# Optimization experiments

Measured on AMD Instinct MI355X. Metric: run time of the kernel, lower is better.

The kernel has to match this reference:

```python
import jax, jax.numpy as jnp
import numpy as np
import math

B, S, D = 4, 2048, 768
H, DH = 12, 64  # num heads, head dim; H*DH == D


def setup_inputs() -> dict:
    key = jax.random.key(0)
    ks = jax.random.split(key, 10)
    q = jax.random.normal(ks[0], (B, S, D), jnp.float32)
    k = jax.random.normal(ks[1], (B, S, D), jnp.float32)
    v = jax.random.normal(ks[2], (B, S, D), jnp.float32)
    attention_mask = jax.random.bernoulli(ks[3], 0.1, (B, S, S))
    s = 1.0 / math.sqrt(D)
    # Linear weights stored as [in, out] so projection is x @ W + b
    Wq = jax.random.uniform(ks[4], (D, D), jnp.float32, -s, s)
    bq = jax.random.uniform(ks[5], (D,), jnp.float32, -s, s)
    Wk = jax.random.uniform(ks[6], (D, D), jnp.float32, -s, s)
    bk = jax.random.uniform(ks[7], (D,), jnp.float32, -s, s)
    Wv = jax.random.uniform(ks[8], (D, D), jnp.float32, -s, s)
    bv = jax.random.uniform(ks[9], (D,), jnp.float32, -s, s)
    return {"q": q, "k": k, "v": v, "attention_mask": attention_mask,
            "Wq": Wq, "bq": bq, "Wk": Wk, "bk": bk, "Wv": Wv, "bv": bv}


def _split_heads(x):
    # [B, S, D] -> [B, H, S, DH]
    return x.reshape(B, -1, H, DH).transpose(0, 2, 1, 3)


def reference(q, k, v, attention_mask, Wq, bq, Wk, bk, Wv, bv):
    Q = _split_heads(q @ Wq + bq)
    K = _split_heads(k @ Wk + bk)
    V = _split_heads(v @ Wv + bv)
    scores = jnp.einsum('bhqd,bhkd->bhqk', Q, K) / math.sqrt(DH)
    # masked_fill(mask, -1e9); 3-dim mask broadcasts over heads
    scores = jnp.where(attention_mask[:, None, :, :], -1.0e9, scores)
    probs = jax.nn.softmax(scores, axis=-1)
    ctx = jnp.einsum('bhqk,bhkd->bhqd', probs, V)
    ctx = ctx.transpose(0, 2, 1, 3).reshape(B, -1, H * DH)
    return ctx, probs
```

## Files before the change

kernel.cpp:

```cpp
#include <hip/hip_runtime.h>
#include <hip/hip_bf16.h>

#define BB 4
#define SS 2048
#define DD 768
#define HH 12
#define NE 6291456

typedef unsigned short u16t;
typedef unsigned char  u8t;
typedef unsigned int   u32t;
typedef __attribute__((ext_vector_type(8)))  short bf16x8;
typedef __attribute__((ext_vector_type(4)))  float f32x4;

union FragU { bf16x8 v; ushort4 h[2]; uint4 u; u32t g[4]; };

__device__ __forceinline__ u16t f2bf(float f) {
  union { float fv; u32t u; } x; x.fv = f;
  u32t r = x.u + 0x7FFFu + ((x.u >> 16) & 1u);
  return (u16t)(r >> 16);
}

__device__ __forceinline__ u32t pkbf2(float a, float b) {
  __hip_bfloat162 h2 = __float22bfloat162_rn(make_float2(a, b));
  union { __hip_bfloat162 h; u32t u; } c; c.h = h2;
  return c.u;
}

__device__ __forceinline__ u32t pack4(u32t w) {
  return ((w & 0x01010101u) * 0x01020408u) >> 24;
}
__device__ __forceinline__ u32t pack16b(uint4 v) {
  return pack4(v.x) | (pack4(v.y) << 4) | (pack4(v.z) << 8) | (pack4(v.w) << 12);
}
__device__ __forceinline__ u32t pack_i4(int4 v) {
  return (v.x ? 1u : 0u) | ((v.y ? 1u : 0u) << 1) | ((v.z ? 1u : 0u) << 2) | ((v.w ? 1u : 0u) << 3);
}
__device__ __forceinline__ u32t pack_f4(float4 v) {
  return (v.x != 0.f ? 1u : 0u) | ((v.y != 0.f ? 1u : 0u) << 1) |
         ((v.z != 0.f ? 1u : 0u) << 2) | ((v.w != 0.f ? 1u : 0u) << 3);
}

__global__ void detect_kernel(const u32t* __restrict__ mp, int* __restrict__ flag)
{
  __shared__ int s_isb, s_isf;
  if (threadIdx.x == 0) { s_isb = 0; s_isf = 0; }
  __syncthreads();
  int isb = 0, isf = 0;
  for (int i = threadIdx.x; i < 16384; i += 256) {
    u32t v = mp[i];
    if ((v & 0xFF000000u) == 0x3F000000u) isf = 1;
    else if (v & 0xFFFFFF00u) isb = 1;
  }
  if (isb) atomicOr(&s_isb, 1);
  if (isf) atomicOr(&s_isf, 1);
  __syncthreads();
  if (threadIdx.x == 0) *flag = s_isf ? 2 : (s_isb ? 1 : 0);
}

__global__ __launch_bounds__(256)
void mask_pack_kernel(const void* __restrict__ msk, const int* __restrict__ flagp,
                      u32t* __restrict__ pm)
{
  const int gid = blockIdx.x * 256 + threadIdx.x;
  const int row = gid >> 6, c = gid & 63;
  const int fmt = *flagp;
  const size_t src = (size_t)(row >> 11) * SS * SS + (size_t)(row & 2047) * SS + c * 32;
  u32t bits;
  if (fmt == 1) {
    const uint4* s = (const uint4*)((const u8t*)msk + src);
    bits = pack16b(s[0]) | (pack16b(s[1]) << 16);
  } else if (fmt == 0) {
    const int4* s = (const int4*)((const int*)msk + src);
    bits = 0;
#pragma unroll
    for (int j = 0; j < 8; ++j) bits |= pack_i4(s[j]) << (j * 4);
  } else {
    const float4* s = (const float4*)((const float*)msk + src);
    bits = 0;
#pragma unroll
    for (int j = 0; j < 8; ++j) bits |= pack_f4(s[j]) << (j * 4);
  }
  pm[(size_t)row * 64 + c] = bits;
}

__global__ __launch_bounds__(256)
void cvt_x_kernel(const float* __restrict__ q, const float* __restrict__ k,
                  const float* __restrict__ v, u16t* __restrict__ xb)
{
  const float* src = (blockIdx.y == 0) ? q : (blockIdx.y == 1) ? k : v;
  u16t* dst = xb + (size_t)blockIdx.y * NE;
  const size_t i = ((size_t)blockIdx.x * 256 + threadIdx.x) * 8;
  float4 f0 = *(const float4*)(src + i);
  float4 f1 = *(const float4*)(src + i + 4);
  uint4 o;
  o.x = pkbf2(f0.x, f0.y); o.y = pkbf2(f0.z, f0.w);
  o.z = pkbf2(f1.x, f1.y); o.w = pkbf2(f1.z, f1.w);
  *(uint4*)(dst + i) = o;
}

__global__ __launch_bounds__(256)
void cvt_w_kernel(const float* __restrict__ Wq, const float* __restrict__ Wk,
                  const float* __restrict__ Wv, u16t* __restrict__ Wt)
{
  __shared__ u16t T[64 * 72];
  const int t = threadIdx.x;
  const float* W = (blockIdx.z == 0) ? Wq : (blockIdx.z == 1) ? Wk : Wv;
  u16t* wt = Wt + (size_t)blockIdx.z * DD * DD;
  const int n0 = blockIdx.x * 64, k0 = blockIdx.y * 64;
  const int r = t >> 2, cs = (t & 3) * 16;
#pragma unroll
  for (int i = 0; i < 4; ++i) {
    float4 f = *(const float4*)(W + (size_t)(k0 + r) * DD + n0 + cs + i * 4);
    T[(cs + i * 4 + 0) * 72 + r] = f2bf(f.x);
    T[(cs + i * 4 + 1) * 72 + r] = f2bf(f.y);
    T[(cs + i * 4 + 2) * 72 + r] = f2bf(f.z);
    T[(cs + i * 4 + 3) * 72 + r] = f2bf(f.w);
  }
  __syncthreads();
#pragma unroll
  for (int i = 0; i < 2; ++i) {
    uint4 vv = *(const uint4*)&T[r * 72 + cs + i * 8];
    *(uint4*)(wt + (size_t)(n0 + r) * DD + k0 + cs + i * 8) = vv;
  }
}

__device__ __forceinline__ void proj_core(const u16t* __restrict__ Xrow,
    const u16t* __restrict__ Wrow, u16t* __restrict__ Ab, u16t* __restrict__ Bb,
    int t, f32x4 acc[8])
{
  const int w = t >> 6, l = t & 63;
  const int lq = l & 15, lg = l >> 4;
  const int gr = l >> 3;
  const int gc = ((l & 7) ^ (l >> 3)) * 8;

#define PSTAGE_A(kk_, buf_)                                                       \
  _Pragma("unroll")                                                               \
  for (int j = 0; j < 2; ++j) {                                                   \
    const int rr = (w * 2 + j) * 8 + gr;                                          \
    const u16t* gsrc = Xrow + (size_t)rr * DD + (kk_) + gc;                       \
    __builtin_amdgcn_global_load_lds(                                             \
        (const __attribute__((address_space(1))) void*)gsrc,                      \
        (__attribute__((address_space(3))) void*)(Ab + (buf_) * 4096 + (w * 2 + j) * 512), \
        16, 0, 0);                                                                \
  }
#define PSTAGE_B(kk_, buf_)                                                       \
  _Pragma("unroll")                                                               \
  for (int j = 0; j < 4; ++j) {                                                   \
    const int rr = (w * 4 + j) * 8 + gr;                                          \
    const u16t* gsrc = Wrow + (size_t)rr * DD + (kk_) + gc;                       \
    __builtin_amdgcn_global_load_lds(                                             \
        (const __attribute__((address_space(1))) void*)gsrc,                      \
        (__attribute__((address_space(3))) void*)(Bb + (buf_) * 8192 + (w * 4 + j) * 512), \
        16, 0, 0);                                                                \
  }

  PSTAGE_A(0, 0)
  PSTAGE_B(0, 0)
  __syncthreads();

  const int xa = (lq & 7) * 8;
  for (int kki = 0; kki < 12; ++kki) {
    const int buf = kki & 1;
    if (kki < 11) { PSTAGE_A((kki + 1) * 64, buf ^ 1) PSTAGE_B((kki + 1) * 64, buf ^ 1) }
    const int arow = w * 16 + lq;
    FragU af[2];
#pragma unroll
    for (int ks = 0; ks < 2; ++ks) {
      af[ks].h[0] = *(const ushort4*)&Ab[buf * 4096 + arow * 64 + ((ks * 32 + 4 * lg) ^ xa)];
      af[ks].h[1] = *(const ushort4*)&Ab[buf * 4096 + arow * 64 + ((ks * 32 + 4 * lg + 16) ^ xa)];
    }
#pragma unroll
    for (int nt = 0; nt < 8; ++nt) {
      const int brow = nt * 16 + lq;
#pragma unroll
      for (int ks = 0; ks < 2; ++ks) {
        FragU bf;
        bf.h[0] = *(const ushort4*)&Bb[buf * 8192 + brow * 64 + ((ks * 32 + 4 * lg) ^ xa)];
        bf.h[1] = *(const ushort4*)&Bb[buf * 8192 + brow * 64 + ((ks * 32 + 4 * lg + 16) ^ xa)];
        acc[nt] = __builtin_amdgcn_mfma_f32_16x16x32_bf16(af[ks].v, bf.v, acc[nt], 0, 0, 0);
      }
    }
    __syncthreads();
  }
#undef PSTAGE_A
#undef PSTAGE_B
}

__global__ __launch_bounds__(256, 3)
void proj_all_kernel(const u16t* __restrict__ Xb, const u16t* __restrict__ Wt,
                     const float* __restrict__ bq, const float* __restrict__ bk,
                     const float* __restrict__ bv,
                     u16t* __restrict__ Qb, u16t* __restrict__ Kb, u16t* __restrict__ Vb)
{
  __shared__ u16t Ab[2 * 4096];
  __shared__ u16t Bb[2 * 8192];
  const int t = threadIdx.x;
  const int w = t >> 6, l = t & 63;
  const int lq = l & 15, lg = l >> 4;
  const int m0 = blockIdx.x * 64;
  const int n0 = blockIdx.y * 128;
  const int z = blockIdx.z;
  const int b = m0 >> 11;

  const float* bias = (z == 0) ? bq : (z == 1) ? bk : bv;
  u16t* out = (z == 0) ? Qb : (z == 1) ? Kb : Vb;

  f32x4 acc[8];
#pragma unroll
  for (int i = 0; i < 8; ++i)
#pragma unroll
    for (int r = 0; r < 4; ++r) acc[i][r] = 0.f;

  proj_core(Xb + (size_t)z * NE + (size_t)m0 * DD,
            Wt + (size_t)z * DD * DD + (size_t)n0 * DD, Ab, Bb, t, acc);

  if (z < 2) {
#pragma unroll
    for (int nt = 0; nt < 8; ++nt) {
      const int n = n0 + nt * 16 + lq;
      const int h = n >> 6, dh = n & 63;
      const float bb = bias[n];
#pragma unroll
      for (int r = 0; r < 4; ++r) {
        const int s = (m0 & 2047) + w * 16 + 4 * lg + r;
        out[((size_t)(b * HH + h) * SS + s) * 64 + dh] = f2bf(acc[nt][r] + bb);
      }
    }
  } else {
    u16t* Tl = Bb;
#pragma unroll
    for (int nt = 0; nt < 8; ++nt) {
      const float bb = bias[n0 + nt * 16 + lq];
#pragma unroll
      for (int r = 0; r < 4; ++r)
        Tl[(nt * 16 + lq) * 72 + w * 16 + 4 * lg + r] = f2bf(acc[nt][r] + bb);
    }
    __syncthreads();
    const int rowl = t >> 1;
    const int half = t & 1;
    const int ncol = n0 + rowl;
    const int h = ncol >> 6, dh = ncol & 63;
    const int s = (m0 & 2047) + half * 32;
    u16t* dst = out + ((size_t)(b * HH + h) * 64 + dh) * SS + s;
#pragma unroll
    for (int i = 0; i < 4; ++i) {
      uint4 vv = *(const uint4*)&Tl[rowl * 72 + half * 32 + i * 8];
      *(uint4*)(dst + i * 8) = vv;
    }
  }
}

__global__ __launch_bounds__(256, 4)
void attn_kernel(const u16t* __restrict__ Qh, const u16t* __restrict__ Kh,
                 const u16t* __restrict__ Vh, const u32t* __restrict__ pm,
                 float* __restrict__ ctx, float* __restrict__ probs)
{
  __shared__ u16t KV[4][64 * 64];

  const int t = threadIdx.x;
  const int w = t >> 6, l = t & 63;
  const int lq = l & 15, lg = l >> 4;

  const int bid = (int)blockIdx.x;
  const int lid = (bid & 7) * 192 + (bid >> 3);
  const int bh = lid >> 5;
  const int qt = lid & 31;
  const int b = bh / HH;
  const int qbase = qt * 64 + w * 16;

  const u16t* qh = Qh + (size_t)bh * SS * 64;
  const u16t* kh = Kh + (size_t)bh * SS * 64;
  const u16t* vh = Vh + (size_t)bh * SS * 64;

  FragU bq_[2];
  {
    const u16t* qp = qh + (size_t)(qbase + lq) * 64;
#pragma unroll
    for (int ks = 0; ks < 2; ++ks) {
      bq_[ks].h[0] = *(const ushort4*)(qp + ks * 32 + 4 * lg);
      bq_[ks].h[1] = *(const ushort4*)(qp + ks * 32 + 4 * lg + 16);
    }
  }

  const u32t* mrow = pm + ((size_t)b * SS + qbase + lq) * 64;

  const float SC = 0.125f * 1.44269504f;
  const float B4 = 4.0f * 1.44269504f;

  const int gr = l >> 3;
  const int gc = ((l & 7) ^ (l >> 3)) * 8;

#define STAGE_K(kt_, slot_)                                                       \
  _Pragma("unroll")                                                               \
  for (int j = 0; j < 2; ++j) {                                                   \
    const int rr = (w * 2 + j) * 8 + gr;                                          \
    const u16t* gsrc = kh + (size_t)((kt_) * 64 + rr) * 64 + gc;                  \
    __builtin_amdgcn_global_load_lds(                                             \
        (const __attribute__((address_space(1))) void*)gsrc,                      \
        (__attribute__((address_space(3))) void*)(&KV[slot_][(w * 2 + j) * 512]), \
        16, 0, 0);                                                                \
  }

#define STAGE_V(kt_, vbuf_)                                                       \
  _Pragma("unroll")                                                               \
  for (int j = 0; j < 2; ++j) {                                                   \
    const int dv = (w * 2 + j) * 8 + gr;                                          \
    const u16t* gsrc = vh + (size_t)dv * SS + (kt_) * 64 + gc;                    \
    __builtin_amdgcn_global_load_lds(                                             \
        (const __attribute__((address_space(1))) void*)gsrc,                      \
        (__attribute__((address_space(3))) void*)(&KV[2 + (vbuf_)][(w * 2 + j) * 512]), \
        16, 0, 0);                                                                \
  }

#define QKT_CHUNK(nt_, slot_, accv)                                               \
  {                                                                               \
    const int krow = (nt_) * 16 + lq;                                             \
    const int xr = (lq & 7) * 8;                                                  \
    _Pragma("unroll")                                                             \
    for (int r = 0; r < 4; ++r) (accv)[r] = 0.f;                                  \
    _Pragma("unroll")                                                             \
    for (int ks = 0; ks < 2; ++ks) {                                              \
      FragU ak;                                                                   \
      ak.h[0] = *(const ushort4*)&KV[slot_][krow * 64 + ((ks * 32 + 4 * lg) ^ xr)]; \
      ak.h[1] = *(const ushort4*)&KV[slot_][krow * 64 + ((ks * 32 + 4 * lg + 16) ^ xr)]; \
      (accv) = __builtin_amdgcn_mfma_f32_16x16x32_bf16(ak.v, bq_[ks].v, (accv), 0, 0, 0); \
    }                                                                             \
  }

#define COMPUTE1(slot_, mw_)                                                      \
  {                                                                               \
    _Pragma("unroll")                                                             \
    for (int nt = 0; nt < 4; ++nt) {                                              \
      f32x4 a;                                                                    \
      QKT_CHUNK(nt, slot_, a)                                                     \
      const u32t word = (nt < 2) ? (mw_).x : (mw_).y;                             \
      const int sh = 16 * (nt & 1) + 4 * lg;                                      \
      _Pragma("unroll")                                                           \
      for (int r = 0; r < 4; ++r) {                                               \
        float s = fmaf(a[r], SC, -B4);                                            \
        if ((word >> (sh + r)) & 1) s = -1.0e9f;                                  \
        ssum += __builtin_exp2f(s);                                               \
      }                                                                           \
    }                                                                             \
  }

  float ssum = 0.f;

  STAGE_K(0, 0)
  uint2 mA = *(const uint2*)(mrow + 0);
  STAGE_K(1, 1)
  uint2 mB = *(const uint2*)(mrow + 2);

  for (int kt = 0; kt < 32; kt += 2) {
    if (kt == 0) { asm volatile("s_waitcnt vmcnt(0)" ::: "memory"); }
    else         { asm volatile("s_waitcnt vmcnt(3)" ::: "memory"); }
    __builtin_amdgcn_s_barrier();
    {
      uint2 mw = mA;
      if (kt < 30) { STAGE_K(kt + 2, (kt + 2) % 3) mA = *(const uint2*)(mrow + (kt + 2) * 2); }
      COMPUTE1(kt % 3, mw)
    }
    if (kt == 0 || kt == 30) { asm volatile("s_waitcnt vmcnt(0)" ::: "memory"); }
    else                     { asm volatile("s_waitcnt vmcnt(3)" ::: "memory"); }
    __builtin_amdgcn_s_barrier();
    {
      uint2 mw = mB;
      if (kt < 30) { STAGE_K(kt + 3, (kt + 3) % 3) mB = *(const uint2*)(mrow + (kt + 3) * 2); }
      COMPUTE1((kt + 1) % 3, mw)
    }
  }

  ssum += __shfl_xor(ssum, 16);
  ssum += __shfl_xor(ssum, 32);
  const float inv = 1.0f / ssum;

  f32x4 acco[4];
#pragma unroll
  for (int i = 0; i < 4; ++i)
#pragma unroll
    for (int r = 0; r < 4; ++r) acco[i][r] = 0.f;

  const size_t prow = ((size_t)bh * SS + qbase + lq) * SS;

  __builtin_amdgcn_s_barrier();
  STAGE_K(0, 0) STAGE_V(0, 0)
  uint2 mw2 = *(const uint2*)(mrow + 0);

  for (int kt = 0; kt < 32; ++kt) {
    const int buf = kt & 1;
    if (kt == 0) { asm volatile("s_waitcnt vmcnt(0)" ::: "memory"); }
    else         { asm volatile("s_waitcnt vmcnt(4)" ::: "memory"); }
    __builtin_amdgcn_s_barrier();
    uint2 mw = mw2;
    if (kt < 31) {
      STAGE_K(kt + 1, buf ^ 1) STAGE_V(kt + 1, buf ^ 1)
      mw2 = *(const uint2*)(mrow + (kt + 1) * 2);
    }

    f32x4 sc[4];
#pragma unroll
    for (int nt = 0; nt < 4; ++nt) {
      f32x4 a;
      QKT_CHUNK(nt, buf, a)
      const u32t word = (nt < 2) ? mw.x : mw.y;
      const int sh = 16 * (nt & 1) + 4 * lg;
#pragma unroll
      for (int r = 0; r < 4; ++r) {
        float s = fmaf(a[r], SC, -B4);
        if ((word >> (sh + r)) & 1) s = -1.0e9f;
        sc[nt][r] = __builtin_exp2f(s) * inv;
      }
    }

#pragma unroll
    for (int nt = 0; nt < 4; ++nt) {
      __builtin_nontemporal_store(sc[nt], (f32x4*)(probs + prow + kt * 64 + nt * 16 + 4 * lg));
    }

    FragU pf[2];
#pragma unroll
    for (int c = 0; c < 2; ++c) {
      pf[c].g[0] = pkbf2(sc[2 * c][0],     sc[2 * c][1]);
      pf[c].g[1] = pkbf2(sc[2 * c][2],     sc[2 * c][3]);
      pf[c].g[2] = pkbf2(sc[2 * c + 1][0], sc[2 * c + 1][1]);
      pf[c].g[3] = pkbf2(sc[2 * c + 1][2], sc[2 * c + 1][3]);
    }

    __builtin_amdgcn_s_setprio(1);
#pragma unroll
    for (int c = 0; c < 2; ++c) {
#pragma unroll
      for (int n0 = 0; n0 < 4; ++n0) {
        const int dv = n0 * 16 + lq;
        const int xv = (lq & 7) * 8;
        FragU bvv;
        bvv.h[0] = *(const ushort4*)&KV[2 + buf][dv * 64 + ((c * 32 + 4 * lg) ^ xv)];
        bvv.h[1] = *(const ushort4*)&KV[2 + buf][dv * 64 + ((c * 32 + 4 * lg + 16) ^ xv)];
        acco[n0] = __builtin_amdgcn_mfma_f32_16x16x32_bf16(pf[c].v, bvv.v, acco[n0], 0, 0, 0);
      }
    }
    __builtin_amdgcn_s_setprio(0);
  }

  {
    const int h = bh % HH;
    const size_t cbase = (size_t)(b * SS + qbase) * DD + h * 64;
#pragma unroll
    for (int n0 = 0; n0 < 4; ++n0)
#pragma unroll
      for (int r = 0; r < 4; ++r)
        ctx[cbase + (size_t)(4 * lg + r) * DD + n0 * 16 + lq] = acco[n0][r];
  }
#undef STAGE_K
#undef STAGE_V
#undef QKT_CHUNK
#undef COMPUTE1
}

extern "C" void kernel_launch(void* const* d_in, const int* in_sizes, int n_in,
                              void* d_out, int out_size, void* d_ws, size_t ws_size,
                              hipStream_t stream)
{
  const float* q   = (const float*)d_in[0];
  const float* k   = (const float*)d_in[1];
  const float* v   = (const float*)d_in[2];
  const void*  msk = d_in[3];
  const float* Wq  = (const float*)d_in[4];
  const float* bq  = (const float*)d_in[5];
  const float* Wk  = (const float*)d_in[6];
  const float* bk  = (const float*)d_in[7];
  const float* Wv  = (const float*)d_in[8];
  const float* bv  = (const float*)d_in[9];
  (void)in_sizes; (void)n_in; (void)out_size; (void)ws_size;

  u16t* Qb = (u16t*)d_ws;
  u16t* Kb = Qb + NE;
  u16t* Vb = Kb + NE;
  u32t* pm = (u32t*)(Vb + NE);
  int* flag = (int*)(pm + (size_t)BB * SS * 64);

  float* ctx   = (float*)d_out;
  float* probs = ctx + NE;

  u16t* Xb = (u16t*)probs;
  u16t* Wt = Xb + (size_t)3 * NE;

  detect_kernel<<<1, 256, 0, stream>>>((const u32t*)msk, flag);
  mask_pack_kernel<<<2048, 256, 0, stream>>>(msk, flag, pm);

  cvt_x_kernel<<<dim3(3072, 3), 256, 0, stream>>>(q, k, v, Xb);
  cvt_w_kernel<<<dim3(12, 12, 3), 256, 0, stream>>>(Wq, Wk, Wv, Wt);

  proj_all_kernel<<<dim3(BB * SS / 64, DD / 128, 3), 256, 0, stream>>>(
      Xb, Wt, bq, bk, bv, Qb, Kb, Vb);

  attn_kernel<<<dim3(1536), 256, 0, stream>>>(Qb, Kb, Vb, pm, ctx, probs);
}
```

Before: 382.8 us.

## Split attention into separate row-sum and PV kernels, use regular probs stores

Splits the single attention kernel into two launches. The first computes the softmax denominators using a 3-slot K-only LDS buffer and writes inverse sums to workspace. The second reloads them and does the normalized probs write plus the PV matmul. The intent is to let each kernel use fewer resources or schedule better, at the cost of an extra launch and a small global round trip for the sums. The probs stores also change from nontemporal to regular stores.

```diff
diff --git a/kernel.cpp b/kernel.cpp
--- a/kernel.cpp
+++ b/kernel.cpp
@@ -251,12 +251,12 @@
   }
 }
 
+
 __global__ __launch_bounds__(256, 4)
-void attn_kernel(const u16t* __restrict__ Qh, const u16t* __restrict__ Kh,
-                 const u16t* __restrict__ Vh, const u32t* __restrict__ pm,
-                 float* __restrict__ ctx, float* __restrict__ probs)
-{
-  __shared__ u16t KV[4][64 * 64];
+void attn_sum_kernel(const u16t* __restrict__ Qh, const u16t* __restrict__ Kh,
+                     const u32t* __restrict__ pm, float* __restrict__ invb)
+{
+  __shared__ u16t KV[3][64 * 64];
 
   const int t = threadIdx.x;
   const int w = t >> 6, l = t & 63;
@@ -271,7 +271,6 @@
 
   const u16t* qh = Qh + (size_t)bh * SS * 64;
   const u16t* kh = Kh + (size_t)bh * SS * 64;
-  const u16t* vh = Vh + (size_t)bh * SS * 64;
 
   FragU bq_[2];
   {
@@ -284,14 +283,12 @@
   }
 
   const u32t* mrow = pm + ((size_t)b * SS + qbase + lq) * 64;
-
   const float SC = 0.125f * 1.44269504f;
   const float B4 = 4.0f * 1.44269504f;
-
   const int gr = l >> 3;
   const int gc = ((l & 7) ^ (l >> 3)) * 8;
 
-#define STAGE_K(kt_, slot_)                                                       \
+#define STAGE_K1(kt_, slot_)                                                      \
   _Pragma("unroll")                                                               \
   for (int j = 0; j < 2; ++j) {                                                   \
     const int rr = (w * 2 + j) * 8 + gr;                                          \
@@ -302,18 +299,7 @@
         16, 0, 0);                                                                \
   }
 
-#define STAGE_V(kt_, vbuf_)                                                       \
-  _Pragma("unroll")                                                               \
-  for (int j = 0; j < 2; ++j) {                                                   \
-    const int dv = (w * 2 + j) * 8 + gr;                                          \
-    const u16t* gsrc = vh + (size_t)dv * SS + (kt_) * 64 + gc;                    \
-    __builtin_amdgcn_global_load_lds(                                             \
-        (const __attribute__((address_space(1))) void*)gsrc,                      \
-        (__attribute__((address_space(3))) void*)(&KV[2 + (vbuf_)][(w * 2 + j) * 512]), \
-        16, 0, 0);                                                                \
-  }
-
-#define QKT_CHUNK(nt_, slot_, accv)                                               \
+#define QKT1(nt_, slot_, accv)                                                    \
   {                                                                               \
     const int krow = (nt_) * 16 + lq;                                             \
     const int xr = (lq & 7) * 8;                                                  \
@@ -333,7 +319,7 @@
     _Pragma("unroll")                                                             \
     for (int nt = 0; nt < 4; ++nt) {                                              \
       f32x4 a;                                                                    \
-      QKT_CHUNK(nt, slot_, a)                                                     \
+      QKT1(nt, slot_, a)                                                          \
       const u32t word = (nt < 2) ? (mw_).x : (mw_).y;                             \
       const int sh = 16 * (nt & 1) + 4 * lg;                                      \
       _Pragma("unroll")                                                           \
@@ -347,9 +333,9 @@
 
   float ssum = 0.f;
 
-  STAGE_K(0, 0)
+  STAGE_K1(0, 0)
   uint2 mA = *(const uint2*)(mrow + 0);
-  STAGE_K(1, 1)
+  STAGE_K1(1, 1)
   uint2 mB = *(const uint2*)(mrow + 2);
 
   for (int kt = 0; kt < 32; kt += 2) {
@@ -358,7 +344,7 @@
     __builtin_amdgcn_s_barrier();
     {
       uint2 mw = mA;
-      if (kt < 30) { STAGE_K(kt + 2, (kt + 2) % 3) mA = *(const uint2*)(mrow + (kt + 2) * 2); }
+      if (kt < 30) { STAGE_K1(kt + 2, (kt + 2) % 3) mA = *(const uint2*)(mrow + (kt + 2) * 2); }
       COMPUTE1(kt % 3, mw)
     }
     if (kt == 0 || kt == 30) { asm volatile("s_waitcnt vmcnt(0)" ::: "memory"); }
@@ -366,14 +352,97 @@
     __builtin_amdgcn_s_barrier();
     {
       uint2 mw = mB;
-      if (kt < 30) { STAGE_K(kt + 3, (kt + 3) % 3) mB = *(const uint2*)(mrow + (kt + 3) * 2); }
+      if (kt < 30) { STAGE_K1(kt + 3, (kt + 3) % 3) mB = *(const uint2*)(mrow + (kt + 3) * 2); }
       COMPUTE1((kt + 1) % 3, mw)
     }
   }
 
   ssum += __shfl_xor(ssum, 16);
   ssum += __shfl_xor(ssum, 32);
-  const float inv = 1.0f / ssum;
+  if (lg == 0)
+    invb[(size_t)bh * SS + qbase + lq] = 1.0f / ssum;
+#undef STAGE_K1
+#undef QKT1
+#undef COMPUTE1
+}
+
+__global__ __launch_bounds__(256, 4)
+void attn_pv_kernel(const u16t* __restrict__ Qh, const u16t* __restrict__ Kh,
+                    const u16t* __restrict__ Vh, const u32t* __restrict__ pm,
+                    const float* __restrict__ invb,
+                    float* __restrict__ ctx, float* __restrict__ probs)
+{
+  __shared__ u16t KV[4][64 * 64];
+
+  const int t = threadIdx.x;
+  const int w = t >> 6, l = t & 63;
+  const int lq = l & 15, lg = l >> 4;
+
+  const int bid = (int)blockIdx.x;
+  const int lid = (bid & 7) * 192 + (bid >> 3);
+  const int bh = lid >> 5;
+  const int qt = lid & 31;
+  const int b = bh / HH;
+  const int qbase = qt * 64 + w * 16;
+
+  const u16t* qh = Qh + (size_t)bh * SS * 64;
+  const u16t* kh = Kh + (size_t)bh * SS * 64;
+  const u16t* vh = Vh + (size_t)bh * SS * 64;
+
+  FragU bq_[2];
+  {
+    const u16t* qp = qh + (size_t)(qbase + lq) * 64;
+#pragma unroll
+    for (int ks = 0; ks < 2; ++ks) {
+      bq_[ks].h[0] = *(const ushort4*)(qp + ks * 32 + 4 * lg);
+      bq_[ks].h[1] = *(const ushort4*)(qp + ks * 32 + 4 * lg + 16);
+    }
+  }
+
+  const float inv = invb[(size_t)bh * SS + qbase + lq];
+
+  const u32t* mrow = pm + ((size_t)b * SS + qbase + lq) * 64;
+  const float SC = 0.125f * 1.44269504f;
+  const float B4 = 4.0f * 1.44269504f;
+  const int gr = l >> 3;
+  const int gc = ((l & 7) ^ (l >> 3)) * 8;
+
+#define STAGE_K2(kt_, buf_)                                                       \
+  _Pragma("unroll")                                                               \
+  for (int j = 0; j < 2; ++j) {                                                   \
+    const int rr = (w * 2 + j) * 8 + gr;                                          \
+    const u16t* gsrc = kh + (size_t)((kt_) * 64 + rr) * 64 + gc;                  \
+    __builtin_amdgcn_global_load_lds(                                             \
+        (const __attribute__((address_space(1))) void*)gsrc,                      \
+        (__attribute__((address_space(3))) void*)(&KV[buf_][(w * 2 + j) * 512]),  \
+        16, 0, 0);                                                                \
+  }
+
+#define STAGE_V2(kt_, buf_)                                                       \
+  _Pragma("unroll")                                                               \
+  for (int j = 0; j < 2; ++j) {                                                   \
+    const int dv = (w * 2 + j) * 8 + gr;                                          \
+    const u16t* gsrc = vh + (size_t)dv * SS + (kt_) * 64 + gc;                    \
+    __builtin_amdgcn_global_load_lds(                                             \
+        (const __attribute__((address_space(1))) void*)gsrc,                      \
+        (__attribute__((address_space(3))) void*)(&KV[2 + (buf_)][(w * 2 + j) * 512]), \
+        16, 0, 0);                                                                \
+  }
+
+#define QKT2(nt_, buf_, accv)                                                     \
+  {                                                                               \
+    const int krow = (nt_) * 16 + lq;                                             \
+    const int xr = (lq & 7) * 8;                                                  \
+    _Pragma("unroll")                                                             \
+    for (int r = 0; r < 4; ++r) (accv)[r] = 0.f;                                  \
+    _Pragma("unroll")                                                             \
+    for (int ks = 0; ks < 2; ++ks) {                                              \
+      FragU ak;                                                                   \
+      ak.h[0] = *(const ushort4*)&KV[buf_][krow * 64 + ((ks * 32 + 4 * lg) ^ xr)]; \
+      ak.h[1] = *(const ushort4*)&KV[buf_][krow * 64 + ((ks * 32 + 4 * lg + 16) ^ xr)]; \
+      (accv) = __builtin_amdgcn_mfma_f32_16x16x32_bf16(ak.v, bq_[ks].v, (accv), 0, 0, 0); \
+    }                                                                             \
+  }
 
   f32x4 acco[4];
 #pragma unroll
@@ -383,8 +452,7 @@
 
   const size_t prow = ((size_t)bh * SS + qbase + lq) * SS;
 
-  __builtin_amdgcn_s_barrier();
-  STAGE_K(0, 0) STAGE_V(0, 0)
+  STAGE_K2(0, 0) STAGE_V2(0, 0)
   uint2 mw2 = *(const uint2*)(mrow + 0);
 
   for (int kt = 0; kt < 32; ++kt) {
@@ -394,7 +462,7 @@
     __builtin_amdgcn_s_barrier();
     uint2 mw = mw2;
     if (kt < 31) {
-      STAGE_K(kt + 1, buf ^ 1) STAGE_V(kt + 1, buf ^ 1)
+      STAGE_K2(kt + 1, buf ^ 1) STAGE_V2(kt + 1, buf ^ 1)
       mw2 = *(const uint2*)(mrow + (kt + 1) * 2);
     }
 
@@ -402,7 +470,7 @@
 #pragma unroll
     for (int nt = 0; nt < 4; ++nt) {
       f32x4 a;
-      QKT_CHUNK(nt, buf, a)
+      QKT2(nt, buf, a)
       const u32t word = (nt < 2) ? mw.x : mw.y;
       const int sh = 16 * (nt & 1) + 4 * lg;
 #pragma unroll
@@ -415,7 +483,7 @@
 
 #pragma unroll
     for (int nt = 0; nt < 4; ++nt) {
-      __builtin_nontemporal_store(sc[nt], (f32x4*)(probs + prow + kt * 64 + nt * 16 + 4 * lg));
+      *(f32x4*)(probs + prow + kt * 64 + nt * 16 + 4 * lg) = sc[nt];
     }
 
     FragU pf[2];
@@ -452,10 +520,9 @@
       for (int r = 0; r < 4; ++r)
         ctx[cbase + (size_t)(4 * lg + r) * DD + n0 * 16 + lq] = acco[n0][r];
   }
-#undef STAGE_K
-#undef STAGE_V
-#undef QKT_CHUNK
-#undef COMPUTE1
+#undef STAGE_K2
+#undef STAGE_V2
+#undef QKT2
 }
 
 extern "C" void kernel_launch(void* const* d_in, const int* in_sizes, int n_in,
@@ -478,7 +545,8 @@
   u16t* Kb = Qb + NE;
   u16t* Vb = Kb + NE;
   u32t* pm = (u32t*)(Vb + NE);
-  int* flag = (int*)(pm + (size_t)BB * SS * 64);
+  float* invb = (float*)(pm + (size_t)BB * SS * 64);
+  int* flag = (int*)(invb + (size_t)BB * HH * SS);
 
   float* ctx   = (float*)d_out;
   float* probs = ctx + NE;
@@ -495,5 +563,6 @@
   proj_all_kernel<<<dim3(BB * SS / 64, DD / 128, 3), 256, 0, stream>>>(
       Xb, Wt, bq, bk, bv, Qb, Kb, Vb);
 
-  attn_kernel<<<dim3(1536), 256, 0, stream>>>(Qb, Kb, Vb, pm, ctx, probs);
-}
+  attn_sum_kernel<<<dim3(1536), 256, 0, stream>>>(Qb, Kb, pm, invb);
+  attn_pv_kernel <<<dim3(1536), 256, 0, stream>>>(Qb, Kb, Vb, pm, invb, ctx, probs);
+}
```

After: 543.3 us. 41.9% more time.

## Process two 16-row query groups per wave to double K/V tile reuse

Applied to the files above, without the earlier changes.

Each wave now handles 32 query rows (two 16-row groups) instead of 16, so a block covers 128 queries and the grid halves to 768 blocks. Each K/V tile staged into LDS is reused by twice as many MFMAs, which halves global K/V traffic and staging per unit of work. Launch bounds drop to 3 waves per SIMD to make room for the doubled accumulators and Q fragments, and the vmcnt waits are adjusted for the extra mask loads. The cost is lower occupancy and fewer blocks to spread across CUs, and the kernel is likely limited by the large probs output write.

```diff
diff --git a/kernel.cpp b/kernel.cpp
--- a/kernel.cpp
+++ b/kernel.cpp
@@ -251,7 +251,7 @@
   }
 }
 
-__global__ __launch_bounds__(256, 4)
+__global__ __launch_bounds__(256, 3)
 void attn_kernel(const u16t* __restrict__ Qh, const u16t* __restrict__ Kh,
                  const u16t* __restrict__ Vh, const u32t* __restrict__ pm,
                  float* __restrict__ ctx, float* __restrict__ probs)
@@ -263,27 +263,29 @@
   const int lq = l & 15, lg = l >> 4;
 
   const int bid = (int)blockIdx.x;
-  const int lid = (bid & 7) * 192 + (bid >> 3);
-  const int bh = lid >> 5;
-  const int qt = lid & 31;
+  const int lid = (bid & 7) * 96 + (bid >> 3);
+  const int bh = lid >> 4;
+  const int qt = lid & 15;
   const int b = bh / HH;
-  const int qbase = qt * 64 + w * 16;
+  const int qbase = qt * 128 + w * 32;
 
   const u16t* qh = Qh + (size_t)bh * SS * 64;
   const u16t* kh = Kh + (size_t)bh * SS * 64;
   const u16t* vh = Vh + (size_t)bh * SS * 64;
 
-  FragU bq_[2];
-  {
-    const u16t* qp = qh + (size_t)(qbase + lq) * 64;
+  FragU bq_[2][2];
+#pragma unroll
+  for (int g = 0; g < 2; ++g) {
+    const u16t* qp = qh + (size_t)(qbase + g * 16 + lq) * 64;
 #pragma unroll
     for (int ks = 0; ks < 2; ++ks) {
-      bq_[ks].h[0] = *(const ushort4*)(qp + ks * 32 + 4 * lg);
-      bq_[ks].h[1] = *(const ushort4*)(qp + ks * 32 + 4 * lg + 16);
-    }
-  }
-
-  const u32t* mrow = pm + ((size_t)b * SS + qbase + lq) * 64;
+      bq_[g][ks].h[0] = *(const ushort4*)(qp + ks * 32 + 4 * lg);
+      bq_[g][ks].h[1] = *(const ushort4*)(qp + ks * 32 + 4 * lg + 16);
+    }
+  }
+
+  const u32t* mrow0 = pm + ((size_t)b * SS + qbase + lq) * 64;
+  const u32t* mrow1 = mrow0 + 16 * 64;
 
   const float SC = 0.125f * 1.44269504f;
   const float B4 = 4.0f * 1.44269504f;
@@ -313,7 +315,7 @@
         16, 0, 0);                                                                \
   }
 
-#define QKT_CHUNK(nt_, slot_, accv)                                               \
+#define QKT_CHUNK(nt_, slot_, g_, accv)                                           \
   {                                                                               \
     const int krow = (nt_) * 16 + lq;                                             \
     const int xr = (lq & 7) * 8;                                                  \
@@ -324,133 +326,205 @@
       FragU ak;                                                                   \
       ak.h[0] = *(const ushort4*)&KV[slot_][krow * 64 + ((ks * 32 + 4 * lg) ^ xr)]; \
       ak.h[1] = *(const ushort4*)&KV[slot_][krow * 64 + ((ks * 32 + 4 * lg + 16) ^ xr)]; \
-      (accv) = __builtin_amdgcn_mfma_f32_16x16x32_bf16(ak.v, bq_[ks].v, (accv), 0, 0, 0); \
+      (accv) = __builtin_amdgcn_mfma_f32_16x16x32_bf16(ak.v, bq_[g_][ks].v, (accv), 0, 0, 0); \
     }                                                                             \
   }
 
-#define COMPUTE1(slot_, mw_)                                                      \
+#define COMPUTE1(slot_, m0_, m1_)                                                 \
   {                                                                               \
     _Pragma("unroll")                                                             \
     for (int nt = 0; nt < 4; ++nt) {                                              \
       f32x4 a;                                                                    \
-      QKT_CHUNK(nt, slot_, a)                                                     \
-      const u32t word = (nt < 2) ? (mw_).x : (mw_).y;                             \
+      QKT_CHUNK(nt, slot_, 0, a)                                                  \
+      const u32t word = (nt < 2) ? (m0_).x : (m0_).y;                             \
       const int sh = 16 * (nt & 1) + 4 * lg;                                      \
       _Pragma("unroll")                                                           \
       for (int r = 0; r < 4; ++r) {                                               \
         float s = fmaf(a[r], SC, -B4);                                            \
         if ((word >> (sh + r)) & 1) s = -1.0e9f;                                  \
-        ssum += __builtin_exp2f(s);                                               \
+        ssum0 += __builtin_exp2f(s);                                              \
       }                                                                           \
     }                                                                             \
-  }
-
-  float ssum = 0.f;
+    _Pragma("unroll")                                                             \
+    for (int nt = 0; nt < 4; ++nt) {                                              \
+      f32x4 a;                                                                    \
+      QKT_CHUNK(nt, slot_, 1, a)                                                  \
+      const u32t word = (nt < 2) ? (m1_).x : (m1_).y;                             \
+      const int sh = 16 * (nt & 1) + 4 * lg;                                      \
+      _Pragma("unroll")                                                           \
+      for (int r = 0; r < 4; ++r) {                                               \
+        float s = fmaf(a[r], SC, -B4);                                            \
+        if ((word >> (sh + r)) & 1) s = -1.0e9f;                                  \
+        ssum1 += __builtin_exp2f(s);                                              \
+      }                                                                           \
+    }                                                                             \
+  }
+
+  float ssum0 = 0.f, ssum1 = 0.f;
 
   STAGE_K(0, 0)
-  uint2 mA = *(const uint2*)(mrow + 0);
+  uint2 mA0 = *(const uint2*)(mrow0 + 0);
+  uint2 mA1 = *(const uint2*)(mrow1 + 0);
   STAGE_K(1, 1)
-  uint2 mB = *(const uint2*)(mrow + 2);
+  uint2 mB0 = *(const uint2*)(mrow0 + 2);
+  uint2 mB1 = *(const uint2*)(mrow1 + 2);
 
   for (int kt = 0; kt < 32; kt += 2) {
-    if (kt == 0) { asm volatile("s_waitcnt vmcnt(0)" ::: "memory"); }
-    else         { asm volatile("s_waitcnt vmcnt(3)" ::: "memory"); }
+    asm volatile("s_waitcnt vmcnt(4)" ::: "memory");
     __builtin_amdgcn_s_barrier();
     {
-      uint2 mw = mA;
-      if (kt < 30) { STAGE_K(kt + 2, (kt + 2) % 3) mA = *(const uint2*)(mrow + (kt + 2) * 2); }
-      COMPUTE1(kt % 3, mw)
-    }
-    if (kt == 0 || kt == 30) { asm volatile("s_waitcnt vmcnt(0)" ::: "memory"); }
-    else                     { asm volatile("s_waitcnt vmcnt(3)" ::: "memory"); }
+      uint2 m0 = mA0, m1 = mA1;
+      if (kt < 30) {
+        STAGE_K(kt + 2, (kt + 2) % 3)
+        mA0 = *(const uint2*)(mrow0 + (kt + 2) * 2);
+        mA1 = *(const uint2*)(mrow1 + (kt + 2) * 2);
+      }
+      COMPUTE1(kt % 3, m0, m1)
+    }
+    if (kt == 30) { asm volatile("s_waitcnt vmcnt(0)" ::: "memory"); }
+    else          { asm volatile("s_waitcnt vmcnt(4)" ::: "memory"); }
     __builtin_amdgcn_s_barrier();
     {
-      uint2 mw = mB;
-      if (kt < 30) { STAGE_K(kt + 3, (kt + 3) % 3) mB = *(const uint2*)(mrow + (kt + 3) * 2); }
-      COMPUTE1((kt + 1) % 3, mw)
-    }
-  }
-
-  ssum += __shfl_xor(ssum, 16);
-  ssum += __shfl_xor(ssum, 32);
-  const float inv = 1.0f / ssum;
-
-  f32x4 acco[4];
-#pragma unroll
-  for (int i = 0; i < 4; ++i)
-#pragma unroll
-    for (int r = 0; r < 4; ++r) acco[i][r] = 0.f;
-
-  const size_t prow = ((size_t)bh * SS + qbase + lq) * SS;
+      uint2 m0 = mB0, m1 = mB1;
+      if (kt < 30) {
+        STAGE_K(kt + 3, (kt + 3) % 3)
+        mB0 = *(const uint2*)(mrow0 + (kt + 3) * 2);
+        mB1 = *(const uint2*)(mrow1 + (kt + 3) * 2);
+      }
+      COMPUTE1((kt + 1) % 3, m0, m1)
+    }
+  }
+
+  ssum0 += __shfl_xor(ssum0, 16);
+  ssum0 += __shfl_xor(ssum0, 32);
+  ssum1 += __shfl_xor(ssum1, 16);
+  ssum1 += __shfl_xor(ssum1, 32);
+  const float inv0 = 1.0f / ssum0;
+  const float inv1 = 1.0f / ssum1;
+
+  f32x4 acco[2][4];
+#pragma unroll
+  for (int g = 0; g < 2; ++g)
+#pragma unroll
+    for (int i = 0; i < 4; ++i)
+#pragma unroll
+      for (int r = 0; r < 4; ++r) acco[g][i][r] = 0.f;
+
+  const size_t prow0 = ((size_t)bh * SS + qbase + lq) * SS;
+  const size_t prow1 = prow0 + (size_t)16 * SS;
 
   __builtin_amdgcn_s_barrier();
   STAGE_K(0, 0) STAGE_V(0, 0)
-  uint2 mw2 = *(const uint2*)(mrow + 0);
+  uint2 mw20 = *(const uint2*)(mrow0 + 0);
+  uint2 mw21 = *(const uint2*)(mrow1 + 0);
 
   for (int kt = 0; kt < 32; ++kt) {
     const int buf = kt & 1;
     if (kt == 0) { asm volatile("s_waitcnt vmcnt(0)" ::: "memory"); }
-    else         { asm volatile("s_waitcnt vmcnt(4)" ::: "memory"); }
+    else         { asm volatile("s_waitcnt vmcnt(8)" ::: "memory"); }
     __builtin_amdgcn_s_barrier();
-    uint2 mw = mw2;
+    uint2 m0 = mw20, m1 = mw21;
     if (kt < 31) {
       STAGE_K(kt + 1, buf ^ 1) STAGE_V(kt + 1, buf ^ 1)
-      mw2 = *(const uint2*)(mrow + (kt + 1) * 2);
-    }
-
-    f32x4 sc[4];
-#pragma unroll
-    for (int nt = 0; nt < 4; ++nt) {
-      f32x4 a;
-      QKT_CHUNK(nt, buf, a)
-      const u32t word = (nt < 2) ? mw.x : mw.y;
-      const int sh = 16 * (nt & 1) + 4 * lg;
-#pragma unroll
-      for (int r = 0; r < 4; ++r) {
-        float s = fmaf(a[r], SC, -B4);
-        if ((word >> (sh + r)) & 1) s = -1.0e9f;
-        sc[nt][r] = __builtin_exp2f(s) * inv;
-      }
-    }
-
-#pragma unroll
-    for (int nt = 0; nt < 4; ++nt) {
-      __builtin_nontemporal_store(sc[nt], (f32x4*)(probs + prow + kt * 64 + nt * 16 + 4 * lg));
-    }
-
-    FragU pf[2];
-#pragma unroll
-    for (int c = 0; c < 2; ++c) {
-      pf[c].g[0] = pkbf2(sc[2 * c][0],     sc[2 * c][1]);
-      pf[c].g[1] = pkbf2(sc[2 * c][2],     sc[2 * c][3]);
-      pf[c].g[2] = pkbf2(sc[2 * c + 1][0], sc[2 * c + 1][1]);
-      pf[c].g[3] = pkbf2(sc[2 * c + 1][2], sc[2 * c + 1][3]);
-    }
-
-    __builtin_amdgcn_s_setprio(1);
-#pragma unroll
-    for (int c = 0; c < 2; ++c) {
-#pragma unroll
-      for (int n0 = 0; n0 < 4; ++n0) {
-        const int dv = n0 * 16 + lq;
-        const int xv = (lq & 7) * 8;
-        FragU bvv;
-        bvv.h[0] = *(const ushort4*)&KV[2 + buf][dv * 64 + ((c * 32 + 4 * lg) ^ xv)];
-        bvv.h[1] = *(const ushort4*)&KV[2 + buf][dv * 64 + ((c * 32 + 4 * lg + 16) ^ xv)];
-        acco[n0] = __builtin_amdgcn_mfma_f32_16x16x32_bf16(pf[c].v, bvv.v, acco[n0], 0, 0, 0);
-      }
-    }
-    __builtin_amdgcn_s_setprio(0);
+      mw20 = *(const uint2*)(mrow0 + (kt + 1) * 2);
+      mw21 = *(const uint2*)(mrow1 + (kt + 1) * 2);
+    }
+
+    {
+      f32x4 sc[4];
+#pragma unroll
+      for (int nt = 0; nt < 4; ++nt) {
+        f32x4 a;
+        QKT_CHUNK(nt, buf, 0, a)
+        const u32t word = (nt < 2) ? m0.x : m0.y;
+        const int sh = 16 * (nt & 1) + 4 * lg;
+#pragma unroll
+        for (int r = 0; r < 4; ++r) {
+          float s = fmaf(a[r], SC, -B4);
+          if ((word >> (sh + r)) & 1) s = -1.0e9f;
+          sc[nt][r] = __builtin_exp2f(s) * inv0;
+        }
+      }
+#pragma unroll
+      for (int nt = 0; nt < 4; ++nt)
+        __builtin_nontemporal_store(sc[nt], (f32x4*)(probs + prow0 + kt * 64 + nt * 16 + 4 * lg));
+      FragU pf[2];
+#pragma unroll
+      for (int c = 0; c < 2; ++c) {
+        pf[c].g[0] = pkbf2(sc[2 * c][0],     sc[2 * c][1]);
+        pf[c].g[1] = pkbf2(sc[2 * c][2],     sc[2 * c][3]);
+        pf[c].g[2] = pkbf2(sc[2 * c + 1][0], sc[2 * c + 1][1]);
+        pf[c].g[3] = pkbf2(sc[2 * c + 1][2], sc[2 * c + 1][3]);
+      }
+      __builtin_amdgcn_s_setprio(1);
+#pragma unroll
+      for (int c = 0; c < 2; ++c) {
+#pragma unroll
+        for (int n0 = 0; n0 < 4; ++n0) {
+          const int dv = n0 * 16 + lq;
+          const int xv = (lq & 7) * 8;
+          FragU bvv;
+          bvv.h[0] = *(const ushort4*)&KV[2 + buf][dv * 64 + ((c * 32 + 4 * lg) ^ xv)];
+          bvv.h[1] = *(const ushort4*)&KV[2 + buf][dv * 64 + ((c * 32 + 4 * lg + 16) ^ xv)];
+          acco[0][n0] = __builtin_amdgcn_mfma_f32_16x16x32_bf16(pf[c].v, bvv.v, acco[0][n0], 0, 0, 0);
+        }
+      }
+      __builtin_amdgcn_s_setprio(0);
+    }
+    {
+      f32x4 sc[4];
+#pragma unroll
+      for (int nt = 0; nt < 4; ++nt) {
+        f32x4 a;
+        QKT_CHUNK(nt, buf, 1, a)
+        const u32t word = (nt < 2) ? m1.x : m1.y;
+        const int sh = 16 * (nt & 1) + 4 * lg;
+#pragma unroll
+        for (int r = 0; r < 4; ++r) {
+          float s = fmaf(a[r], SC, -B4);
+          if ((word >> (sh + r)) & 1) s = -1.0e9f;
+          sc[nt][r] = __builtin_exp2f(s) * inv1;
+        }
+      }
+#pragma unroll
+      for (int nt = 0; nt < 4; ++nt)
+        __builtin_nontemporal_store(sc[nt], (f32x4*)(probs + prow1 + kt * 64 + nt * 16 + 4 * lg));
+      FragU pf[2];
+#pragma unroll
+      for (int c = 0; c < 2; ++c) {
+        pf[c].g[0] = pkbf2(sc[2 * c][0],     sc[2 * c][1]);
+        pf[c].g[1] = pkbf2(sc[2 * c][2],     sc[2 * c][3]);
+        pf[c].g[2] = pkbf2(sc[2 * c + 1][0], sc[2 * c + 1][1]);
+        pf[c].g[3] = pkbf2(sc[2 * c + 1][2], sc[2 * c + 1][3]);
+      }
+      __builtin_amdgcn_s_setprio(1);
+#pragma unroll
+      for (int c = 0; c < 2; ++c) {
+#pragma unroll
+        for (int n0 = 0; n0 < 4; ++n0) {
+          const int dv = n0 * 16 + lq;
+          const int xv = (lq & 7) * 8;
+          FragU bvv;
+          bvv.h[0] = *(const ushort4*)&KV[2 + buf][dv * 64 + ((c * 32 + 4 * lg) ^ xv)];
+          bvv.h[1] = *(const ushort4*)&KV[2 + buf][dv * 64 + ((c * 32 + 4 * lg + 16) ^ xv)];
+          acco[1][n0] = __builtin_amdgcn_mfma_f32_16x16x32_bf16(pf[c].v, bvv.v, acco[1][n0], 0, 0, 0);
+        }
+      }
+      __builtin_amdgcn_s_setprio(0);
+    }
   }
 
   {
     const int h = bh % HH;
-    const size_t cbase = (size_t)(b * SS + qbase) * DD + h * 64;
-#pragma unroll
-    for (int n0 = 0; n0 < 4; ++n0)
-#pragma unroll
-      for (int r = 0; r < 4; ++r)
-        ctx[cbase + (size_t)(4 * lg + r) * DD + n0 * 16 + lq] = acco[n0][r];
+#pragma unroll
+    for (int g = 0; g < 2; ++g) {
+      const size_t cbase = (size_t)(b * SS + qbase + g * 16) * DD + h * 64;
+#pragma unroll
+      for (int n0 = 0; n0 < 4; ++n0)
+#pragma unroll
+        for (int r = 0; r < 4; ++r)
+          ctx[cbase + (size_t)(4 * lg + r) * DD + n0 * 16 + lq] = acco[g][n0][r];
+    }
   }
 #undef STAGE_K
 #undef STAGE_V
@@ -495,5 +569,5 @@
   proj_all_kernel<<<dim3(BB * SS / 64, DD / 128, 3), 256, 0, stream>>>(
       Xb, Wt, bq, bk, bv, Qb, Kb, Vb);
 
-  attn_kernel<<<dim3(1536), 256, 0, stream>>>(Qb, Kb, Vb, pm, ctx, probs);
-}
+  attn_kernel<<<dim3(768), 256, 0, stream>>>(Qb, Kb, Vb, pm, ctx, probs);
+}
```

Measured after the change: 412.6 us. 7.8% more time.
